# Optimization experiments

Hardware: AMD Instinct MI355X
Metric: run time of the kernel (lower is better)

## Reference

```python
import jax, jax.numpy as jnp
import numpy as np

B, N, H, E = 32, 256, 128, 16

def setup_inputs() -> dict:
    key = jax.random.key(0)
    k1, k2, k3, k4, k5, k6, k7, k8 = jax.random.split(key, 8)
    h = jax.random.normal(k1, (B, N, H), dtype=jnp.float32)
    edge_attr = jax.random.normal(k2, (B, N, N, E), dtype=jnp.float32)
    adj = jax.random.randint(k3, (B, N, N), 0, 2, dtype=jnp.int32)
    num_nodes = jax.random.randint(k4, (B,), 0, N).astype(jnp.int64)
    # Linear W: in = H + E, out = H (torch convention: y = x @ W.T + b)
    lim_w = 1.0 / np.sqrt(H + E)
    W_w = jax.random.uniform(k5, (H, H + E), jnp.float32, -lim_w, lim_w)
    W_b = jax.random.uniform(k6, (H,), jnp.float32, -lim_w, lim_w)
    lim_u = 1.0 / np.sqrt(H)
    U_w = jax.random.uniform(k7, (H, H), jnp.float32, -lim_u, lim_u)
    U_b = jax.random.uniform(k8, (H,), jnp.float32, -lim_u, lim_u)
    return {"h": h, "edge_attr": edge_attr, "adj": adj, "num_nodes": num_nodes,
            "W_w": W_w, "W_b": W_b, "U_w": U_w, "U_b": U_b}

def reference(h, edge_attr, adj, num_nodes, W_w, W_b, U_w, U_b):
    batch, max_nodes, hidden = h.shape
    # gate[i,j] = 1 if adj[:, i, j].sum() > 0  (condition is over the whole batch,
    # and the message is then added for ALL batch elements — matches the torch loop)
    gate = (adj.sum(axis=0) > 0).astype(h.dtype)            # [N, N]
    # Split W into hidden and edge blocks: W(cat(h_i, e_ij)) = h_i Wh^T + e_ij We^T + b
    Wh = W_w[:, :hidden]                                    # [H, H]
    We = W_w[:, hidden:]                                    # [H, E]
    hW = jnp.einsum('bih,oh->bio', h, Wh)                   # [B, N, H]
    term_h = jnp.einsum('ij,bio->bjo', gate, hW)            # [B, N, H]
    e_sum = jnp.einsum('ij,bije->bje', gate, edge_attr)     # [B, N, E]
    term_e = jnp.einsum('bje,oe->bjo', e_sum, We)           # [B, N, H]
    count = gate.sum(axis=0)                                # [N] — bias added once per active (i,j)
    messages = term_h + term_e + count[None, :, None] * W_b[None, None, :]
    # mask padded nodes
    mask = (jnp.arange(max_nodes)[None, :] < num_nodes[:, None])[..., None]
    messages = messages * mask.astype(h.dtype)
    h_new = jnp.einsum('bnh,oh->bno', h + messages, U_w) + U_b
    return h_new
```

## Files before the change

### kernel.cpp

```cpp
#include <hip/hip_runtime.h>

#define Bn 32
#define Nn 256
#define Hn 128
#define En 16
#define WWC 144
#define JT 8
#define IC 8

typedef float v4 __attribute__((ext_vector_type(4)));

__global__ __launch_bounds__(256) void k_stream(const float* __restrict__ edge, const int* __restrict__ adj,
                                                const float* __restrict__ h, const float* __restrict__ U_w,
                                                float* __restrict__ epart, float* __restrict__ gate,
                                                float* __restrict__ Ppart, float* __restrict__ U_T) {
    int bid = blockIdx.x, t = threadIdx.x;
    __shared__ v4 sred[128];
    if (bid < 2048) {
        int b = bid >> 6, r = bid & 63, ic = r >> 3, jt = r & 7;
        int ig = t >> 7, vc = t & 127;
        const float* p = edge + ((size_t)b << 20) + (size_t)(ic * 32 + ig) * 4096 + jt * 512 + vc * 4;
        v4 a0 = {0.f,0.f,0.f,0.f}, a1 = a0, a2 = a0, a3 = a0;
        #pragma unroll
        for (int k = 0; k < 16; ++k) {
            v4 v = *reinterpret_cast<const v4*>(p + (size_t)k * 8192);
            if ((k & 3) == 0) a0 += v; else if ((k & 3) == 1) a1 += v;
            else if ((k & 3) == 2) a2 += v; else a3 += v;
        }
        v4 s = (a0 + a1) + (a2 + a3);
        if (ig == 1) sred[vc] = s;
        __syncthreads();
        if (ig == 0) {
            s += sred[vc];
            *reinterpret_cast<v4*>(&epart[((size_t)(ic * 32 + b) * JT + jt) * 512 + vc * 4]) = s;
        }
    } else if (bid < 2304) {
        int i = bid - 2048, j = t;
        int s = 0;
        #pragma unroll
        for (int b = 0; b < Bn; ++b) s += adj[(b * Nn + i) * Nn + j];
        gate[i * Nn + j] = (s > 0) ? 1.0f : 0.0f;
    } else if (bid < 2560) {
        int pb = bid - 2304, b = pb >> 3, ic = pb & 7;
        int hh = t & 127, half = t >> 7;
        float* red = reinterpret_cast<float*>(sred);
        float s = 0.f;
        #pragma unroll
        for (int k = 0; k < 16; ++k)
            s += h[((size_t)b * Nn + ic * 32 + half * 16 + k) * Hn + hh];
        red[t] = s;
        __syncthreads();
        if (t < 128) Ppart[(ic * 32 + b) * Hn + t] = red[t] + red[t + 128];
    } else {
        int m = (bid - 2560) * 2 + (t >> 7), o = t & 127;
        U_T[m * Hn + o] = U_w[o * Hn + m];
    }
}

__global__ __launch_bounds__(512) void k_final(
    const float* __restrict__ h, const float* __restrict__ U_T, const float* __restrict__ U_b,
    const float* __restrict__ W_w, const float* __restrict__ W_b, const float* __restrict__ gate,
    const float* __restrict__ Ppart, const float* __restrict__ epart, const float* __restrict__ edge,
    const int* __restrict__ num_nodes, float* __restrict__ out) {
    int jt = blockIdx.x, j0 = jt * 32, b = blockIdx.y, t = threadIdx.x;
    __shared__ float shj[Hn][33];
    __shared__ float sgate[Nn][36];
    __shared__ float sWe[Hn][17];
    __shared__ float sE[32][17];
    __shared__ float sP[Hn], sQ[Hn], sWb[Hn], srbuf[Hn], sesub[En], scnt[32];
    __shared__ int szc[32];

    #pragma unroll
    for (int q = 0; q < 2; ++q) {
        int f = t + 512 * q, j = f >> 5, c = f & 31;
        v4 v = *reinterpret_cast<const v4*>(&h[((size_t)b * Nn + j0 + j) * Hn + c * 4]);
        shj[c * 4 + 0][j] = v[0];
        shj[c * 4 + 1][j] = v[1];
        shj[c * 4 + 2][j] = v[2];
        shj[c * 4 + 3][j] = v[3];
    }
    #pragma unroll
    for (int q = 0; q < 4; ++q) {
        int f = t + 512 * q, i = f >> 3, c = f & 7;
        *reinterpret_cast<v4*>(&sgate[i][c * 4]) =
            *reinterpret_cast<const v4*>(&gate[i * Nn + j0 + c * 4]);
    }
    {
        int m = t >> 2, c = t & 3;
        v4 v = *reinterpret_cast<const v4*>(&W_w[m * WWC + Hn + c * 4]);
        sWe[m][c * 4 + 0] = v[0];
        sWe[m][c * 4 + 1] = v[1];
        sWe[m][c * 4 + 2] = v[2];
        sWe[m][c * 4 + 3] = v[3];
    }
    if (t < 128) {
        v4 s = {0.f,0.f,0.f,0.f};
        #pragma unroll
        for (int ic = 0; ic < IC; ++ic)
            s += *reinterpret_cast<const v4*>(&epart[((size_t)(ic * 32 + b) * JT + jt) * 512 + t * 4]);
        int j = t >> 2, e4 = (t & 3) * 4;
        sE[j][e4 + 0] = s[0]; sE[j][e4 + 1] = s[1]; sE[j][e4 + 2] = s[2]; sE[j][e4 + 3] = s[3];
    } else if (t < 256) {
        int hh = t - 128;
        float p = 0.f;
        #pragma unroll
        for (int ic = 0; ic < IC; ++ic) p += Ppart[(ic * 32 + b) * Hn + hh];
        sP[hh] = p;
    } else if (t < 384) {
        sWb[t - 256] = W_b[t - 256];
    }
    __syncthreads();

    if (t < 128) {
        float s = 0.f;
        #pragma unroll 8
        for (int hh = 0; hh < Hn; ++hh) s += W_w[t * WWC + hh] * sP[hh];
        sQ[t] = s;
    } else if (t < 160) {
        int jj = t - 128, zc = 0;
        for (int i = 0; i < Nn; ++i) zc += (sgate[i][jj] == 0.0f) ? 1 : 0;
        szc[jj] = zc;
        scnt[jj] = (float)(Nn - zc);
    }
    __syncthreads();

    int nn = num_nodes[b];
    for (int jj = 0; jj < 32; ++jj) {
        if (szc[jj] > 0) {
            if (t < 128) {
                float r = 0.f;
                for (int i = 0; i < Nn; ++i)
                    if (sgate[i][jj] == 0.0f) r += h[((size_t)b * Nn + i) * Hn + t];
                srbuf[t] = r;
            } else if (t < 144) {
                int e = t - 128;
                float r = 0.f;
                for (int i = 0; i < Nn; ++i)
                    if (sgate[i][jj] == 0.0f) r += edge[(((size_t)b * Nn + i) * Nn + j0 + jj) * En + e];
                sesub[e] = r;
            }
            __syncthreads();
            if (t < 128 && (j0 + jj) < nn) {
                float c = 0.f;
                #pragma unroll 8
                for (int hh = 0; hh < Hn; ++hh) c += W_w[t * WWC + hh] * srbuf[hh];
                #pragma unroll
                for (int e = 0; e < En; ++e) c += sWe[t][e] * sesub[e];
                shj[t][jj] -= c;
            }
            __syncthreads();
        }
    }

    #pragma unroll
    for (int q = 0; q < 8; ++q) {
        int f = t + 512 * q, m = f >> 5, j = f & 31;
        if (j0 + j < nn) {
            float y = sQ[m] + scnt[j] * sWb[m];
            #pragma unroll
            for (int e = 0; e < En; ++e) y += sWe[m][e] * sE[j][e];
            shj[m][j] += y;
        }
    }
    __syncthreads();

    int og = t & 31, o4 = og * 4, jq = t >> 5, j2 = jq * 2;
    v4 acc0 = {0.f,0.f,0.f,0.f}, acc1 = acc0;
    #pragma unroll 8
    for (int m = 0; m < Hn; ++m) {
        v4 u = *reinterpret_cast<const v4*>(&U_T[m * Hn + o4]);
        acc0 += shj[m][j2] * u;
        acc1 += shj[m][j2 + 1] * u;
    }
    v4 ub = *reinterpret_cast<const v4*>(&U_b[o4]);
    *reinterpret_cast<v4*>(&out[((size_t)b * Nn + j0 + j2) * Hn + o4])     = acc0 + ub;
    *reinterpret_cast<v4*>(&out[((size_t)b * Nn + j0 + j2 + 1) * Hn + o4]) = acc1 + ub;
}

extern "C" void kernel_launch(void* const* d_in, const int* in_sizes, int n_in,
                              void* d_out, int out_size, void* d_ws, size_t ws_size,
                              hipStream_t stream) {
    const float* h    = (const float*)d_in[0];
    const float* edge = (const float*)d_in[1];
    const int*   adj  = (const int*)d_in[2];
    const int*   nn   = (const int*)d_in[3];
    const float* W_w  = (const float*)d_in[4];
    const float* W_b  = (const float*)d_in[5];
    const float* U_w  = (const float*)d_in[6];
    const float* U_b  = (const float*)d_in[7];
    float* out = (float*)d_out;

    float* ws    = (float*)d_ws;
    float* gate  = ws;
    float* Ppart = ws + 65536;
    float* U_T   = ws + 98304;
    float* epart = ws + 114688;

    hipLaunchKernelGGL(k_stream, dim3(2624),   dim3(256), 0, stream,
                       edge, adj, h, U_w, epart, gate, Ppart, U_T);
    hipLaunchKernelGGL(k_final,  dim3(JT, Bn), dim3(512), 0, stream,
                       h, U_T, U_b, W_w, W_b, gate, Ppart, epart, edge, nn, out);
}
```

Measured before the change: 49.02 us.

## Restructure edge reduction into contiguous chunks and vectorize gate computation

The edge_attr streaming reduction now has each block read a contiguous 128KB chunk of rows and write 32 partial sums per (b,jt) without shared-memory reduction. The final kernel then sums 32 partials instead of 8. The adjacency gate is computed with int4 vector loads, four rows per block, which cuts the block count. In k_final the zero-count of gate columns is split across all 512 threads with a two-level reduction instead of 32 serial threads. The aim is fewer blocks, simpler memory access in the bandwidth-bound pass and less serial work, at the cost of a larger partial buffer and more reads in k_final.

```diff
diff --git a/kernel.cpp b/kernel.cpp
--- a/kernel.cpp
+++ b/kernel.cpp
@@ -6,6 +6,7 @@
 #define En 16
 #define WWC 144
 #define JT 8
+#define NC 32
 #define IC 8
 
 typedef float v4 __attribute__((ext_vector_type(4)));
@@ -15,44 +16,49 @@
                                                 float* __restrict__ epart, float* __restrict__ gate,
                                                 float* __restrict__ Ppart, float* __restrict__ U_T) {
     int bid = blockIdx.x, t = threadIdx.x;
-    __shared__ v4 sred[128];
-    if (bid < 2048) {
-        int b = bid >> 6, r = bid & 63, ic = r >> 3, jt = r & 7;
-        int ig = t >> 7, vc = t & 127;
-        const float* p = edge + ((size_t)b << 20) + (size_t)(ic * 32 + ig) * 4096 + jt * 512 + vc * 4;
+    __shared__ float red[256];
+    if (bid < 1024) {
+        int b = bid >> 5, c = bid & 31;
+        const float* base = edge + ((size_t)b << 20) + ((size_t)c << 15) + t * 4;
         v4 a0 = {0.f,0.f,0.f,0.f}, a1 = a0, a2 = a0, a3 = a0;
         #pragma unroll
-        for (int k = 0; k < 16; ++k) {
-            v4 v = *reinterpret_cast<const v4*>(p + (size_t)k * 8192);
-            if ((k & 3) == 0) a0 += v; else if ((k & 3) == 1) a1 += v;
-            else if ((k & 3) == 2) a2 += v; else a3 += v;
-        }
-        v4 s = (a0 + a1) + (a2 + a3);
-        if (ig == 1) sred[vc] = s;
-        __syncthreads();
-        if (ig == 0) {
-            s += sred[vc];
-            *reinterpret_cast<v4*>(&epart[((size_t)(ic * 32 + b) * JT + jt) * 512 + vc * 4]) = s;
-        }
-    } else if (bid < 2304) {
-        int i = bid - 2048, j = t;
-        int s = 0;
-        #pragma unroll
-        for (int b = 0; b < Bn; ++b) s += adj[(b * Nn + i) * Nn + j];
-        gate[i * Nn + j] = (s > 0) ? 1.0f : 0.0f;
-    } else if (bid < 2560) {
-        int pb = bid - 2304, b = pb >> 3, ic = pb & 7;
+        for (int r = 0; r < 8; ++r) {
+            const float* rp = base + r * 4096;
+            a0 += *reinterpret_cast<const v4*>(rp);
+            a1 += *reinterpret_cast<const v4*>(rp + 1024);
+            a2 += *reinterpret_cast<const v4*>(rp + 2048);
+            a3 += *reinterpret_cast<const v4*>(rp + 3072);
+        }
+        int off = (t & 127) * 4, hi = t >> 7;
+        size_t eb = (((size_t)b * JT) * NC + c) * 512 + off;
+        *reinterpret_cast<v4*>(&epart[eb + (size_t)(0 + hi) * (NC * 512)]) = a0;
+        *reinterpret_cast<v4*>(&epart[eb + (size_t)(2 + hi) * (NC * 512)]) = a1;
+        *reinterpret_cast<v4*>(&epart[eb + (size_t)(4 + hi) * (NC * 512)]) = a2;
+        *reinterpret_cast<v4*>(&epart[eb + (size_t)(6 + hi) * (NC * 512)]) = a3;
+    } else if (bid < 1088) {
+        int i0 = (bid - 1024) * 4;
+        int4 s = {0, 0, 0, 0};
+        #pragma unroll
+        for (int b = 0; b < Bn; ++b) {
+            int4 v = *reinterpret_cast<const int4*>(&adj[((size_t)b * Nn + i0) * Nn + t * 4]);
+            s.x += v.x; s.y += v.y; s.z += v.z; s.w += v.w;
+        }
+        v4 g;
+        g[0] = s.x > 0 ? 1.f : 0.f; g[1] = s.y > 0 ? 1.f : 0.f;
+        g[2] = s.z > 0 ? 1.f : 0.f; g[3] = s.w > 0 ? 1.f : 0.f;
+        *reinterpret_cast<v4*>(&gate[i0 * Nn + t * 4]) = g;
+    } else if (bid < 1344) {
+        int pb = bid - 1088, b = pb >> 3, ic = pb & 7;
         int hh = t & 127, half = t >> 7;
-        float* red = reinterpret_cast<float*>(sred);
         float s = 0.f;
         #pragma unroll
         for (int k = 0; k < 16; ++k)
             s += h[((size_t)b * Nn + ic * 32 + half * 16 + k) * Hn + hh];
         red[t] = s;
         __syncthreads();
-        if (t < 128) Ppart[(ic * 32 + b) * Hn + t] = red[t] + red[t + 128];
+        if (t < 128) Ppart[(ic * Bn + b) * Hn + t] = red[t] + red[t + 128];
     } else {
-        int m = (bid - 2560) * 2 + (t >> 7), o = t & 127;
+        int m = (bid - 1344) * 2 + (t >> 7), o = t & 127;
         U_T[m * Hn + o] = U_w[o * Hn + m];
     }
 }
@@ -68,6 +74,7 @@
     __shared__ float sWe[Hn][17];
     __shared__ float sE[32][17];
     __shared__ float sP[Hn], sQ[Hn], sWb[Hn], srbuf[Hn], sesub[En], scnt[32];
+    __shared__ int szp[16][32];
     __shared__ int szc[32];
 
     #pragma unroll
@@ -95,32 +102,42 @@
     }
     if (t < 128) {
         v4 s = {0.f,0.f,0.f,0.f};
-        #pragma unroll
-        for (int ic = 0; ic < IC; ++ic)
-            s += *reinterpret_cast<const v4*>(&epart[((size_t)(ic * 32 + b) * JT + jt) * 512 + t * 4]);
+        const float* ep = epart + (((size_t)b * JT + jt) * NC) * 512 + t * 4;
+        #pragma unroll
+        for (int c2 = 0; c2 < NC; ++c2)
+            s += *reinterpret_cast<const v4*>(ep + c2 * 512);
         int j = t >> 2, e4 = (t & 3) * 4;
         sE[j][e4 + 0] = s[0]; sE[j][e4 + 1] = s[1]; sE[j][e4 + 2] = s[2]; sE[j][e4 + 3] = s[3];
     } else if (t < 256) {
         int hh = t - 128;
         float p = 0.f;
         #pragma unroll
-        for (int ic = 0; ic < IC; ++ic) p += Ppart[(ic * 32 + b) * Hn + hh];
+        for (int ic = 0; ic < IC; ++ic) p += Ppart[(ic * Bn + b) * Hn + hh];
         sP[hh] = p;
     } else if (t < 384) {
         sWb[t - 256] = W_b[t - 256];
     }
     __syncthreads();
 
-    if (t < 128) {
+    {
+        int jj = t & 31, grp = t >> 5, zp = 0;
+        #pragma unroll
+        for (int i = grp; i < Nn; i += 16) zp += (sgate[i][jj] == 0.0f) ? 1 : 0;
+        szp[grp][jj] = zp;
+    }
+    __syncthreads();
+    if (t < 32) {
+        int zc = 0;
+        #pragma unroll
+        for (int g2 = 0; g2 < 16; ++g2) zc += szp[g2][t];
+        szc[t] = zc;
+        scnt[t] = (float)(Nn - zc);
+    } else if (t >= 128 && t < 256) {
+        int m = t - 128;
         float s = 0.f;
         #pragma unroll 8
-        for (int hh = 0; hh < Hn; ++hh) s += W_w[t * WWC + hh] * sP[hh];
-        sQ[t] = s;
-    } else if (t < 160) {
-        int jj = t - 128, zc = 0;
-        for (int i = 0; i < Nn; ++i) zc += (sgate[i][jj] == 0.0f) ? 1 : 0;
-        szc[jj] = zc;
-        scnt[jj] = (float)(Nn - zc);
+        for (int hh = 0; hh < Hn; ++hh) s += W_w[m * WWC + hh] * sP[hh];
+        sQ[m] = s;
     }
     __syncthreads();
 
@@ -196,7 +213,7 @@
     float* U_T   = ws + 98304;
     float* epart = ws + 114688;
 
-    hipLaunchKernelGGL(k_stream, dim3(2624),   dim3(256), 0, stream,
+    hipLaunchKernelGGL(k_stream, dim3(1408),   dim3(256), 0, stream,
                        edge, adj, h, U_w, epart, gate, Ppart, U_T);
     hipLaunchKernelGGL(k_final,  dim3(JT, Bn), dim3(512), 0, stream,
                        h, U_T, U_b, W_w, W_b, gate, Ppart, epart, edge, nn, out);
```

New measurement: 54.77 us. +11.7%, slower.

## Precompute per-column zero-gate counts in stream kernel and drop gate tile from final

Applied to the files above, without the earlier changes.

The adjacency reduction is vectorized to int4 loads, and it now also accumulates per-column zero-gate counts into a global array with atomics, which a memset clears first. The final kernel no longer loads a 256x32 gate tile into shared memory or counts zeros itself. It reads the precomputed counts, and the rare correction path reads gate from global memory. Other changes: nontemporal loads and stores on the streaming edge/adj reads and the output, an epart layout made contiguous per block, and a 4-way split of the W·P matvec. The cost is an extra memset launch and atomics, and the correction loop now does uncached global gate reads.

```diff
diff --git a/kernel.cpp b/kernel.cpp
--- a/kernel.cpp
+++ b/kernel.cpp
@@ -9,21 +9,23 @@
 #define IC 8
 
 typedef float v4 __attribute__((ext_vector_type(4)));
+typedef int   i4 __attribute__((ext_vector_type(4)));
 
 __global__ __launch_bounds__(256) void k_stream(const float* __restrict__ edge, const int* __restrict__ adj,
                                                 const float* __restrict__ h, const float* __restrict__ U_w,
                                                 float* __restrict__ epart, float* __restrict__ gate,
-                                                float* __restrict__ Ppart, float* __restrict__ U_T) {
+                                                float* __restrict__ Ppart, float* __restrict__ U_T,
+                                                int* __restrict__ zcq) {
     int bid = blockIdx.x, t = threadIdx.x;
-    __shared__ v4 sred[128];
     if (bid < 2048) {
         int b = bid >> 6, r = bid & 63, ic = r >> 3, jt = r & 7;
         int ig = t >> 7, vc = t & 127;
+        __shared__ v4 sred[128];
         const float* p = edge + ((size_t)b << 20) + (size_t)(ic * 32 + ig) * 4096 + jt * 512 + vc * 4;
         v4 a0 = {0.f,0.f,0.f,0.f}, a1 = a0, a2 = a0, a3 = a0;
         #pragma unroll
         for (int k = 0; k < 16; ++k) {
-            v4 v = *reinterpret_cast<const v4*>(p + (size_t)k * 8192);
+            v4 v = __builtin_nontemporal_load(reinterpret_cast<const v4*>(p + (size_t)k * 8192));
             if ((k & 3) == 0) a0 += v; else if ((k & 3) == 1) a1 += v;
             else if ((k & 3) == 2) a2 += v; else a3 += v;
         }
@@ -32,27 +34,40 @@
         __syncthreads();
         if (ig == 0) {
             s += sred[vc];
-            *reinterpret_cast<v4*>(&epart[((size_t)(ic * 32 + b) * JT + jt) * 512 + vc * 4]) = s;
-        }
-    } else if (bid < 2304) {
-        int i = bid - 2048, j = t;
-        int s = 0;
-        #pragma unroll
-        for (int b = 0; b < Bn; ++b) s += adj[(b * Nn + i) * Nn + j];
-        gate[i * Nn + j] = (s > 0) ? 1.0f : 0.0f;
-    } else if (bid < 2560) {
-        int pb = bid - 2304, b = pb >> 3, ic = pb & 7;
+            *reinterpret_cast<v4*>(&epart[(((size_t)b * JT + jt) * IC + ic) * 512 + vc * 4]) = s;
+        }
+    } else if (bid < 2112) {
+        int f0 = (bid - 2048) * 1024;
+        i4 s = {0, 0, 0, 0};
+        #pragma unroll
+        for (int b = 0; b < Bn; ++b)
+            s += __builtin_nontemporal_load(reinterpret_cast<const i4*>(&adj[(size_t)b * (Nn * Nn) + f0 + t * 4]));
+        v4 g;
+        g[0] = s[0] > 0 ? 1.f : 0.f; g[1] = s[1] > 0 ? 1.f : 0.f;
+        g[2] = s[2] > 0 ? 1.f : 0.f; g[3] = s[3] > 0 ? 1.f : 0.f;
+        *reinterpret_cast<v4*>(&gate[f0 + t * 4]) = g;
+        __shared__ int szl[4][Nn];
+        int rr = t >> 6, c4 = (t & 63) * 4;
+        szl[rr][c4 + 0] = (s[0] == 0);
+        szl[rr][c4 + 1] = (s[1] == 0);
+        szl[rr][c4 + 2] = (s[2] == 0);
+        szl[rr][c4 + 3] = (s[3] == 0);
+        __syncthreads();
+        int zs = szl[0][t] + szl[1][t] + szl[2][t] + szl[3][t];
+        if (zs > 0) atomicAdd(&zcq[t], zs);
+    } else if (bid < 2368) {
+        int pb = bid - 2112, b = pb >> 3, ic = pb & 7;
         int hh = t & 127, half = t >> 7;
-        float* red = reinterpret_cast<float*>(sred);
+        __shared__ float red[256];
         float s = 0.f;
         #pragma unroll
         for (int k = 0; k < 16; ++k)
             s += h[((size_t)b * Nn + ic * 32 + half * 16 + k) * Hn + hh];
         red[t] = s;
         __syncthreads();
-        if (t < 128) Ppart[(ic * 32 + b) * Hn + t] = red[t] + red[t + 128];
+        if (t < 128) Ppart[(ic * Bn + b) * Hn + t] = red[t] + red[t + 128];
     } else {
-        int m = (bid - 2560) * 2 + (t >> 7), o = t & 127;
+        int m = (bid - 2368) * 2 + (t >> 7), o = t & 127;
         U_T[m * Hn + o] = U_w[o * Hn + m];
     }
 }
@@ -61,14 +76,13 @@
     const float* __restrict__ h, const float* __restrict__ U_T, const float* __restrict__ U_b,
     const float* __restrict__ W_w, const float* __restrict__ W_b, const float* __restrict__ gate,
     const float* __restrict__ Ppart, const float* __restrict__ epart, const float* __restrict__ edge,
-    const int* __restrict__ num_nodes, float* __restrict__ out) {
+    const int* __restrict__ zcq, const int* __restrict__ num_nodes, float* __restrict__ out) {
     int jt = blockIdx.x, j0 = jt * 32, b = blockIdx.y, t = threadIdx.x;
     __shared__ float shj[Hn][33];
-    __shared__ float sgate[Nn][36];
     __shared__ float sWe[Hn][17];
     __shared__ float sE[32][17];
+    __shared__ float sqp[Hn][4];
     __shared__ float sP[Hn], sQ[Hn], sWb[Hn], srbuf[Hn], sesub[En], scnt[32];
-    __shared__ int szc[32];
 
     #pragma unroll
     for (int q = 0; q < 2; ++q) {
@@ -79,12 +93,6 @@
         shj[c * 4 + 2][j] = v[2];
         shj[c * 4 + 3][j] = v[3];
     }
-    #pragma unroll
-    for (int q = 0; q < 4; ++q) {
-        int f = t + 512 * q, i = f >> 3, c = f & 7;
-        *reinterpret_cast<v4*>(&sgate[i][c * 4]) =
-            *reinterpret_cast<const v4*>(&gate[i * Nn + j0 + c * 4]);
-    }
     {
         int m = t >> 2, c = t & 3;
         v4 v = *reinterpret_cast<const v4*>(&W_w[m * WWC + Hn + c * 4]);
@@ -94,49 +102,53 @@
         sWe[m][c * 4 + 3] = v[3];
     }
     if (t < 128) {
+        const float* ep = epart + (((size_t)b * JT + jt) * IC) * 512 + t * 4;
         v4 s = {0.f,0.f,0.f,0.f};
         #pragma unroll
         for (int ic = 0; ic < IC; ++ic)
-            s += *reinterpret_cast<const v4*>(&epart[((size_t)(ic * 32 + b) * JT + jt) * 512 + t * 4]);
+            s += *reinterpret_cast<const v4*>(ep + ic * 512);
         int j = t >> 2, e4 = (t & 3) * 4;
         sE[j][e4 + 0] = s[0]; sE[j][e4 + 1] = s[1]; sE[j][e4 + 2] = s[2]; sE[j][e4 + 3] = s[3];
     } else if (t < 256) {
         int hh = t - 128;
         float p = 0.f;
         #pragma unroll
-        for (int ic = 0; ic < IC; ++ic) p += Ppart[(ic * 32 + b) * Hn + hh];
+        for (int ic = 0; ic < IC; ++ic) p += Ppart[(ic * Bn + b) * Hn + hh];
         sP[hh] = p;
     } else if (t < 384) {
         sWb[t - 256] = W_b[t - 256];
-    }
-    __syncthreads();
-
-    if (t < 128) {
-        float s = 0.f;
-        #pragma unroll 8
-        for (int hh = 0; hh < Hn; ++hh) s += W_w[t * WWC + hh] * sP[hh];
-        sQ[t] = s;
-    } else if (t < 160) {
-        int jj = t - 128, zc = 0;
-        for (int i = 0; i < Nn; ++i) zc += (sgate[i][jj] == 0.0f) ? 1 : 0;
-        szc[jj] = zc;
-        scnt[jj] = (float)(Nn - zc);
-    }
+    } else if (t < 416) {
+        scnt[t - 384] = (float)(Nn - zcq[j0 + t - 384]);
+    }
+    __syncthreads();
+
+    {
+        int m = t >> 2, q = t & 3;
+        const v4* wp = reinterpret_cast<const v4*>(&W_w[m * WWC + q * 32]);
+        const v4* pp = reinterpret_cast<const v4*>(&sP[q * 32]);
+        v4 sv = {0.f,0.f,0.f,0.f};
+        #pragma unroll
+        for (int k = 0; k < 8; ++k) sv += wp[k] * pp[k];
+        sqp[m][q] = (sv[0] + sv[1]) + (sv[2] + sv[3]);
+    }
+    __syncthreads();
+    if (t < 128) sQ[t] = (sqp[t][0] + sqp[t][1]) + (sqp[t][2] + sqp[t][3]);
     __syncthreads();
 
     int nn = num_nodes[b];
     for (int jj = 0; jj < 32; ++jj) {
-        if (szc[jj] > 0) {
+        if (scnt[jj] < 255.5f) {
             if (t < 128) {
                 float r = 0.f;
                 for (int i = 0; i < Nn; ++i)
-                    if (sgate[i][jj] == 0.0f) r += h[((size_t)b * Nn + i) * Hn + t];
+                    if (gate[i * Nn + j0 + jj] == 0.0f) r += h[((size_t)b * Nn + i) * Hn + t];
                 srbuf[t] = r;
             } else if (t < 144) {
                 int e = t - 128;
                 float r = 0.f;
                 for (int i = 0; i < Nn; ++i)
-                    if (sgate[i][jj] == 0.0f) r += edge[(((size_t)b * Nn + i) * Nn + j0 + jj) * En + e];
+                    if (gate[i * Nn + j0 + jj] == 0.0f)
+                        r += edge[(((size_t)b * Nn + i) * Nn + j0 + jj) * En + e];
                 sesub[e] = r;
             }
             __syncthreads();
@@ -173,8 +185,10 @@
         acc1 += shj[m][j2 + 1] * u;
     }
     v4 ub = *reinterpret_cast<const v4*>(&U_b[o4]);
-    *reinterpret_cast<v4*>(&out[((size_t)b * Nn + j0 + j2) * Hn + o4])     = acc0 + ub;
-    *reinterpret_cast<v4*>(&out[((size_t)b * Nn + j0 + j2 + 1) * Hn + o4]) = acc1 + ub;
+    __builtin_nontemporal_store(acc0 + ub,
+        reinterpret_cast<v4*>(&out[((size_t)b * Nn + j0 + j2) * Hn + o4]));
+    __builtin_nontemporal_store(acc1 + ub,
+        reinterpret_cast<v4*>(&out[((size_t)b * Nn + j0 + j2 + 1) * Hn + o4]));
 }
 
 extern "C" void kernel_launch(void* const* d_in, const int* in_sizes, int n_in,
@@ -195,9 +209,11 @@
     float* Ppart = ws + 65536;
     float* U_T   = ws + 98304;
     float* epart = ws + 114688;
-
-    hipLaunchKernelGGL(k_stream, dim3(2624),   dim3(256), 0, stream,
-                       edge, adj, h, U_w, epart, gate, Ppart, U_T);
+    int*   zcq   = (int*)(ws + 114688 + 1048576);
+
+    hipMemsetAsync(zcq, 0, Nn * sizeof(int), stream);
+    hipLaunchKernelGGL(k_stream, dim3(2432),   dim3(256), 0, stream,
+                       edge, adj, h, U_w, epart, gate, Ppart, U_T, zcq);
     hipLaunchKernelGGL(k_final,  dim3(JT, Bn), dim3(512), 0, stream,
-                       h, U_T, U_b, W_w, W_b, gate, Ppart, epart, edge, nn, out);
+                       h, U_T, U_b, W_w, W_b, gate, Ppart, epart, edge, zcq, nn, out);
 }
```

Result: slower. 51.32 us (+4.7%).
